# Kernel optimization log

Measured on AMD Instinct MI355X. Metric: run time of the kernel, lower is better.

## Reference

```python
import jax, jax.numpy as jnp
import numpy as np

T, B, I, H, O = 2048, 128, 128, 512, 128


def setup_inputs() -> dict:
    key = jax.random.key(0)
    ks = jax.random.split(key, 8)
    s = 0.05  # keep tanh out of hard saturation
    return {
        "input_seq": jax.random.randint(ks[0], (T, B), 0, I),
        "emb": jax.random.normal(ks[1], (I, I), jnp.float32),
        "Wxh_w": jax.random.normal(ks[2], (H, I), jnp.float32) * s,
        "Wxh_b": jax.random.normal(ks[3], (H,), jnp.float32) * s,
        "Whh_w": jax.random.normal(ks[4], (H, H), jnp.float32) * s,
        "Whh_b": jax.random.normal(ks[5], (H,), jnp.float32) * s,
        "dec_w": jax.random.normal(ks[6], (O, H), jnp.float32) * s,
        "dec_b": jax.random.normal(ks[7], (O,), jnp.float32) * s,
    }


def reference(input_seq, emb, Wxh_w, Wxh_b, Whh_w, Whh_b, dec_w, dec_b):
    x = emb[input_seq]                                   # [T, B, I]
    # input projection is h-independent: hoist out of the recurrence
    xh = jnp.einsum("tbi,hi->tbh", x, Wxh_w) + Wxh_b    # [T, B, H]

    def step(h, xt):
        # torch: res = tanh(Whh(h) + Wxh(x1)); self.h = res.detach()
        res = jnp.tanh(h @ Whh_w.T + Whh_b + xt)         # [B, H]
        return jax.lax.stop_gradient(res), res

    h0 = jnp.zeros((x.shape[1], Whh_w.shape[0]), x.dtype)
    _, out = jax.lax.scan(step, h0, xh)                  # [T, B, H]
    return out @ dec_w.T + dec_b                         # [T, B, O]
```

## Files before the change

kernel.cpp:

```cpp
#include <hip/hip_runtime.h>


#define TT 2048
#define BB 128
#define HH 512
#define OO 128
#define MAGIC 123456.0f
#define NLDG 18

typedef _Float16 h2_t __attribute__((ext_vector_type(2)));
typedef unsigned int u32x4 __attribute__((ext_vector_type(4)));
union UF { unsigned int u; float f; h2_t h; unsigned short us[2]; };

__device__ __forceinline__ unsigned int packf16(float a, float b) {
  UF r; r.h[0] = (_Float16)a; r.h[1] = (_Float16)b; return r.u;
}
__device__ __forceinline__ float dot2a(unsigned int a, unsigned int b, float c) {
  UF x, y; x.u = a; y.u = b;
#if __has_builtin(__builtin_amdgcn_fdot2)
  return __builtin_amdgcn_fdot2(x.h, y.h, c, false);
#else
  return fmaf((float)x.h[1], (float)y.h[1], fmaf((float)x.h[0], (float)y.h[0], c));
#endif
}
__device__ __forceinline__ unsigned short f16bits(float x) {
  UF r; r.h[0] = (_Float16)x; r.h[1] = (_Float16)0.f; return r.us[0];
}
__device__ __forceinline__ float f16tof(unsigned short u) {
  UF r; r.us[0] = u; r.us[1] = 0; return (float)r.h[0];
}
__device__ __forceinline__ float tanh_fast(float x) {
  float e = __expf(2.0f * x);
  return 1.0f - 2.0f / (e + 1.0f);
}
__device__ __forceinline__ float sanz(float x) {
  return (x >= -1e20f && x <= 1e20f) ? x : 0.f;
}
__device__ __forceinline__ unsigned int rdlane(unsigned int v, int l) {
#if __has_builtin(__builtin_amdgcn_readlane)
  return (unsigned int)__builtin_amdgcn_readlane((int)v, l);
#else
  return (unsigned int)__shfl((int)v, l, 64);
#endif
}

extern "C" __global__ void k_init(float* __restrict__ mk) {
  if (threadIdx.x < 8) mk[threadIdx.x] = 0.f;
}

extern "C" __global__ __launch_bounds__(512)
void k_pre(const float* __restrict__ emb, const float* __restrict__ wxh,
           const float* __restrict__ bxh, const float* __restrict__ bhh,
           float* __restrict__ P, float* __restrict__ mk) {
  const int id = blockIdx.x;
  const int j = threadIdx.x;
  const float4* er = (const float4*)(emb + id * 128);
  const float4* wr = (const float4*)(wxh + j * 128);
  float acc = 0.f;
  #pragma unroll
  for (int c = 0; c < 32; ++c) {
    const float4 e = er[c], w = wr[c];
    acc = fmaf(e.x, w.x, fmaf(e.y, w.y, fmaf(e.z, w.z, fmaf(e.w, w.w, acc))));
  }
  P[id * HH + j] = acc + bxh[j] + bhh[j];
  if (id == 0 && j == 0) mk[0] = MAGIC;
}

extern "C" __global__ __launch_bounds__(256)
void k_pack(const float* __restrict__ whh, unsigned int* __restrict__ wpack) {
  const int row = blockIdx.x;
  const int pd = threadIdx.x;
  const float2 w = *(const float2*)(whh + row * 512 + 2 * pd);
  wpack[row * 256 + pd] = packf16(w.x, w.y);
}

extern "C" __global__ __launch_bounds__(256)
void k_packd(const float* __restrict__ dw, uint4* __restrict__ decP4) {
  const int id = blockIdx.x * 256 + threadIdx.x;
  const int c4 = id >> 7, o = id & 127;
  const float* src = dw + o * 512 + 8 * c4;
  uint4 v;
  v.x = packf16(src[0], src[1]);
  v.y = packf16(src[2], src[3]);
  v.z = packf16(src[4], src[5]);
  v.w = packf16(src[6], src[7]);
  decP4[id] = v;
}

#define LOADBLK7(PTR, W0, W1, W2, W3, W4, W5, W6)             \
  asm volatile(                                               \
    "global_load_dwordx4 %0, %7, off\n\t"                     \
    "global_load_dwordx4 %1, %7, off offset:16\n\t"           \
    "global_load_dwordx4 %2, %7, off offset:32\n\t"           \
    "global_load_dwordx4 %3, %7, off offset:48\n\t"           \
    "global_load_dwordx4 %4, %7, off offset:64\n\t"           \
    "global_load_dwordx4 %5, %7, off offset:80\n\t"           \
    "global_load_dwordx4 %6, %7, off offset:96\n\t"           \
    "s_waitcnt vmcnt(0)"                                      \
    : "=&v"(W0), "=&v"(W1), "=&v"(W2), "=&v"(W3),             \
      "=&v"(W4), "=&v"(W5), "=&v"(W6)                         \
    : "v"(PTR))
#define LOADBLK4(PTR, W0, W1, W2, W3)                         \
  asm volatile(                                               \
    "global_load_dwordx4 %0, %4, off\n\t"                     \
    "global_load_dwordx4 %1, %4, off offset:16\n\t"           \
    "global_load_dwordx4 %2, %4, off offset:32\n\t"           \
    "global_load_dwordx4 %3, %4, off offset:48\n\t"           \
    "s_waitcnt vmcnt(0)"                                      \
    : "=&v"(W0), "=&v"(W1), "=&v"(W2), "=&v"(W3)              \
    : "v"(PTR))

#define GSTEP(W4, g)                                    \
  {                                                     \
    a0 = dot2a((W4).x, rdlane(hv.x, (g)), a0);          \
    a1 = dot2a((W4).y, rdlane(hv.y, (g)), a1);          \
    a2 = dot2a((W4).z, rdlane(hv.z, (g)), a2);          \
    a3 = dot2a((W4).w, rdlane(hv.w, (g)), a3);          \
  }

#define WL(X) \
  X(0) X(1) X(2) X(3) X(4) X(5) X(6) X(7) X(8) X(9) \
  X(10) X(11) X(12) X(13) X(14) X(15) X(16) X(17) X(18) X(19) \
  X(20) X(21) X(22) X(23) X(24) X(25) X(26) X(27) X(28) X(29) \
  X(30) X(31) X(32) X(33) X(34) X(35) X(36) X(37) X(38) X(39) \
  X(40) X(41) X(42) X(43) X(44) X(45)
#define DECLW(i) u32x4 w_##i;
#define USEW(i) GSTEP(w_##i, i)

extern "C" __global__
__attribute__((amdgpu_flat_work_group_size(512, 512), amdgpu_waves_per_eu(2, 2)))
void k_rec(const int* __restrict__ idx, const float* __restrict__ P,
           const unsigned int* __restrict__ wpack,
           float* __restrict__ hstate, unsigned short* __restrict__ ring16,
           float* __restrict__ mk, int t0, int nT) {
  extern __shared__ __align__(16) unsigned char smem[];
  u32x4* wl4 = (u32x4*)smem;
  unsigned short* hb16 = (unsigned short*)(smem + NLDG * 512 * 16);
  const uint4* hb4 = (const uint4*)hb16;
  const int tid = threadIdx.x;
  const int b = blockIdx.x;
  const int lane = tid & 63;
  if (t0 == 0 && b == 0 && tid == 0) mk[1] = MAGIC;

  const u32x4* wp = (const u32x4*)(wpack + (size_t)tid * 256);
  #pragma unroll
  for (int s = 0; s < NLDG; ++s) wl4[s * 512 + tid] = wp[46 + s];

  WL(DECLW)
  LOADBLK7(wp +  0, w_0,  w_1,  w_2,  w_3,  w_4,  w_5,  w_6);
  LOADBLK7(wp +  7, w_7,  w_8,  w_9,  w_10, w_11, w_12, w_13);
  LOADBLK7(wp + 14, w_14, w_15, w_16, w_17, w_18, w_19, w_20);
  LOADBLK7(wp + 21, w_21, w_22, w_23, w_24, w_25, w_26, w_27);
  LOADBLK7(wp + 28, w_28, w_29, w_30, w_31, w_32, w_33, w_34);
  LOADBLK7(wp + 35, w_35, w_36, w_37, w_38, w_39, w_40, w_41);
  LOADBLK4(wp + 42, w_42, w_43, w_44, w_45);

  const float h0 = (t0 == 0) ? 0.f : hstate[b * HH + tid];
  hb16[tid] = f16bits(h0);
  float hlast = h0;
  __syncthreads();

  for (int tl = 0; tl < nT; ++tl) {
    const int rb = tl & 1, wb = rb ^ 1;
    const int id = idx[(t0 + tl) * BB + b];
    const float pj = P[id * HH + tid];
    const uint4 hv = hb4[rb * 64 + lane];
    float a0 = 0.f, a1 = 0.f, a2 = 0.f, a3 = 0.f;
    #pragma unroll
    for (int s = 0; s < NLDG; ++s) {
      const u32x4 w4 = wl4[s * 512 + tid];
      GSTEP(w4, 46 + s);
    }
    WL(USEW)
    float s = a0 + a1 + a2 + a3 + pj;
    s = fminf(fmaxf(s, -30.f), 30.f);
    const float hvf = tanh_fast(s);
    const unsigned short h16 = f16bits(hvf);
    hb16[wb * 512 + tid] = h16;
    ring16[((size_t)tl * BB + b) * HH + tid] = h16;
    hlast = hvf;
    __syncthreads();
  }
  hstate[b * HH + tid] = hlast;
  if (t0 == 0 && b == 0 && tid == 0) mk[2] = MAGIC;
}

extern "C" __global__ __launch_bounds__(512)
void k_chk(const int* __restrict__ idx, const float* __restrict__ P,
           const unsigned int* __restrict__ wpack,
           const unsigned short* __restrict__ ring16, float* __restrict__ mk) {
  __shared__ unsigned short h1s[512];
  const int j = threadIdx.x;
  h1s[j] = ring16[j];
  __syncthreads();
  {
    const float pj = P[idx[0] * HH + j];
    const float s = fminf(fmaxf(pj, -30.f), 30.f);
    const float d = fabsf(f16tof(h1s[j]) - f16tof(f16bits(tanh_fast(s))));
    if (d > 0.02f) mk[5] = 7.f;
  }
  {
    const unsigned int* wr = wpack + (size_t)j * 256;
    const unsigned int* hp = (const unsigned int*)h1s;
    float a0 = 0.f, a1 = 0.f, a2 = 0.f, a3 = 0.f;
    for (int g = 0; g < 64; ++g) {
      a0 = dot2a(wr[4 * g + 0], hp[4 * g + 0], a0);
      a1 = dot2a(wr[4 * g + 1], hp[4 * g + 1], a1);
      a2 = dot2a(wr[4 * g + 2], hp[4 * g + 2], a2);
      a3 = dot2a(wr[4 * g + 3], hp[4 * g + 3], a3);
    }
    const float pj = P[idx[BB] * HH + j];
    const float s = fminf(fmaxf((a0 + a1) + (a2 + a3) + pj, -30.f), 30.f);
    const float d = fabsf(f16tof(ring16[BB * HH + j]) - f16tof(f16bits(tanh_fast(s))));
    if (d > 0.02f) mk[4] = 7.f;
  }
}

extern "C" __global__ __launch_bounds__(512)
void k_dec(const uint4* __restrict__ ring4, const uint4* __restrict__ decP4,
           const float* __restrict__ decb, float* __restrict__ out,
           float* __restrict__ mk, int t0) {
  extern __shared__ __align__(16) unsigned char smem[];
  uint4* hl4 = (uint4*)smem;
  const int tid = threadIdx.x;
  const size_t r0 = (size_t)blockIdx.x * 64;
  #pragma unroll
  for (int i = 0; i < 8; ++i) {
    const int u = i * 512 + tid;
    hl4[u] = ring4[(r0 + (u >> 6)) * 64 + (u & 63)];
  }
  __syncthreads();
  const int oq = tid & 31, tq = tid >> 5;
  float acc[4][4];
  #pragma unroll
  for (int r = 0; r < 4; ++r)
    #pragma unroll
    for (int s = 0; s < 4; ++s) acc[r][s] = 0.f;
  #pragma unroll 2
  for (int c4 = 0; c4 < 64; ++c4) {
    uint4 h4[4], d4[4];
    #pragma unroll
    for (int s = 0; s < 4; ++s) h4[s] = hl4[(tq + 16 * s) * 64 + c4];
    #pragma unroll
    for (int r = 0; r < 4; ++r) d4[r] = decP4[c4 * 128 + oq + 32 * r];
    #pragma unroll
    for (int r = 0; r < 4; ++r)
      #pragma unroll
      for (int s = 0; s < 4; ++s) {
        acc[r][s] = dot2a(d4[r].x, h4[s].x, acc[r][s]);
        acc[r][s] = dot2a(d4[r].y, h4[s].y, acc[r][s]);
        acc[r][s] = dot2a(d4[r].z, h4[s].z, acc[r][s]);
        acc[r][s] = dot2a(d4[r].w, h4[s].w, acc[r][s]);
      }
  }
  #pragma unroll
  for (int r = 0; r < 4; ++r) {
    const float db = decb[oq + 32 * r];
    #pragma unroll
    for (int s = 0; s < 4; ++s) {
      const size_t g = r0 + tq + 16 * s;
      out[((size_t)t0 * BB + g) * OO + oq + 32 * r] = sanz(acc[r][s] + db);
    }
  }
  if (t0 == 0 && blockIdx.x == 0 && tid == 0) mk[3] = MAGIC;
}

extern "C" __global__ void k_probe(const float* __restrict__ mk, float* __restrict__ out,
                                   int wsTooSmall) {
  if (wsTooSmall)     { out[0] = 100000.f; return; }
  if (mk[0] != MAGIC) { out[0] = 200000.f; return; }
  if (mk[1] != MAGIC) { out[0] = 300000.f; return; }
  if (mk[2] != MAGIC) { out[0] = 400000.f; return; }
  if (mk[3] != MAGIC) { out[0] = 500000.f; return; }
  if (mk[5] == 7.f)   { out[0] = 600000.f; return; }
  if (mk[4] == 7.f)   { out[0] = 700000.f; return; }
}

extern "C" void kernel_launch(void* const* d_in, const int* in_sizes, int n_in,
                              void* d_out, int out_size, void* d_ws, size_t ws_size,
                              hipStream_t stream) {
  (void)in_sizes; (void)n_in; (void)out_size;
  const int* idx = (const int*)d_in[0];
  const float* emb = (const float*)d_in[1];
  const float* wxh = (const float*)d_in[2];
  const float* bxh = (const float*)d_in[3];
  const float* whh = (const float*)d_in[4];
  const float* bhh = (const float*)d_in[5];
  const float* dw  = (const float*)d_in[6];
  const float* db  = (const float*)d_in[7];
  float* out = (float*)d_out;

  char* ws = (char*)d_ws;
  float* P = (float*)ws;
  float* hstate = (float*)(ws + (256 << 10));
  float* mk = (float*)(ws + (512 << 10));
  unsigned int* wpack = (unsigned int*)(ws + (516 << 10));
  uint4* decP4 = (uint4*)(ws + (1076 << 10));
  unsigned short* ring16 = (unsigned short*)(ws + (1204 << 10));

  int chunkT = 0;
  const int opts[8] = {2048, 1024, 768, 512, 256, 128, 32, 8};
  for (int i = 0; i < 8; ++i) {
    const size_t need = (size_t)(1204 << 10) + (size_t)opts[i] * BB * HH * 2;
    if (ws_size >= need) { chunkT = opts[i]; break; }
  }
  if (chunkT == 0) {
    k_probe<<<1, 1, 0, stream>>>(nullptr, out, 1);
    return;
  }

  const int ldsRec = NLDG * 512 * 16 + 2048;
  const int ldsDec = 64 * 64 * 16;
  (void)hipFuncSetAttribute(reinterpret_cast<const void*>(k_rec),
                            hipFuncAttributeMaxDynamicSharedMemorySize, ldsRec);
  (void)hipFuncSetAttribute(reinterpret_cast<const void*>(k_dec),
                            hipFuncAttributeMaxDynamicSharedMemorySize, ldsDec);

  k_init<<<1, 64, 0, stream>>>(mk);
  k_pre<<<128, 512, 0, stream>>>(emb, wxh, bxh, bhh, P, mk);
  k_pack<<<512, 256, 0, stream>>>(whh, wpack);
  k_packd<<<32, 256, 0, stream>>>(dw, decP4);
  bool first = true;
  for (int t0 = 0; t0 < TT; t0 += chunkT) {
    k_rec<<<BB, 512, ldsRec, stream>>>(idx, P, wpack, hstate, ring16, mk, t0, chunkT);
    if (first) {
      k_chk<<<1, 512, 0, stream>>>(idx, P, wpack, ring16, mk);
      first = false;
    }
    k_dec<<<chunkT * 2, 512, ldsDec, stream>>>((const uint4*)ring16, decP4, db, out, mk, t0);
  }
  k_probe<<<1, 1, 0, stream>>>(mk, out, 0);
}
```

Before: 4.953 ms.

## Stream recurrent weights from L2 each step instead of holding them in registers

```diff
diff --git a/kernel.cpp b/kernel.cpp
--- a/kernel.cpp
+++ b/kernel.cpp
@@ -6,7 +6,8 @@
 #define HH 512
 #define OO 128
 #define MAGIC 123456.0f
-#define NLDG 18
+#define NLDSG 19
+#define NSTRG 45
 
 typedef _Float16 h2_t __attribute__((ext_vector_type(2)));
 typedef unsigned int u32x4 __attribute__((ext_vector_type(4)));
@@ -72,6 +73,14 @@
   const int pd = threadIdx.x;
   const float2 w = *(const float2*)(whh + row * 512 + 2 * pd);
   wpack[row * 256 + pd] = packf16(w.x, w.y);
+}
+
+extern "C" __global__ __launch_bounds__(512)
+void k_packS(const unsigned int* __restrict__ wpack, u32x4* __restrict__ wstr4) {
+  const int g = blockIdx.x;
+  const int t = threadIdx.x;
+  const u32x4* src = (const u32x4*)wpack + (size_t)t * 64 + g;
+  wstr4[(size_t)g * 512 + t] = *src;
 }
 
 extern "C" __global__ __launch_bounds__(256)
@@ -87,29 +96,6 @@
   decP4[id] = v;
 }
 
-#define LOADBLK7(PTR, W0, W1, W2, W3, W4, W5, W6)             \
-  asm volatile(                                               \
-    "global_load_dwordx4 %0, %7, off\n\t"                     \
-    "global_load_dwordx4 %1, %7, off offset:16\n\t"           \
-    "global_load_dwordx4 %2, %7, off offset:32\n\t"           \
-    "global_load_dwordx4 %3, %7, off offset:48\n\t"           \
-    "global_load_dwordx4 %4, %7, off offset:64\n\t"           \
-    "global_load_dwordx4 %5, %7, off offset:80\n\t"           \
-    "global_load_dwordx4 %6, %7, off offset:96\n\t"           \
-    "s_waitcnt vmcnt(0)"                                      \
-    : "=&v"(W0), "=&v"(W1), "=&v"(W2), "=&v"(W3),             \
-      "=&v"(W4), "=&v"(W5), "=&v"(W6)                         \
-    : "v"(PTR))
-#define LOADBLK4(PTR, W0, W1, W2, W3)                         \
-  asm volatile(                                               \
-    "global_load_dwordx4 %0, %4, off\n\t"                     \
-    "global_load_dwordx4 %1, %4, off offset:16\n\t"           \
-    "global_load_dwordx4 %2, %4, off offset:32\n\t"           \
-    "global_load_dwordx4 %3, %4, off offset:48\n\t"           \
-    "s_waitcnt vmcnt(0)"                                      \
-    : "=&v"(W0), "=&v"(W1), "=&v"(W2), "=&v"(W3)              \
-    : "v"(PTR))
-
 #define GSTEP(W4, g)                                    \
   {                                                     \
     a0 = dot2a((W4).x, rdlane(hv.x, (g)), a0);          \
@@ -118,42 +104,24 @@
     a3 = dot2a((W4).w, rdlane(hv.w, (g)), a3);          \
   }
 
-#define WL(X) \
-  X(0) X(1) X(2) X(3) X(4) X(5) X(6) X(7) X(8) X(9) \
-  X(10) X(11) X(12) X(13) X(14) X(15) X(16) X(17) X(18) X(19) \
-  X(20) X(21) X(22) X(23) X(24) X(25) X(26) X(27) X(28) X(29) \
-  X(30) X(31) X(32) X(33) X(34) X(35) X(36) X(37) X(38) X(39) \
-  X(40) X(41) X(42) X(43) X(44) X(45)
-#define DECLW(i) u32x4 w_##i;
-#define USEW(i) GSTEP(w_##i, i)
-
 extern "C" __global__
 __attribute__((amdgpu_flat_work_group_size(512, 512), amdgpu_waves_per_eu(2, 2)))
 void k_rec(const int* __restrict__ idx, const float* __restrict__ P,
-           const unsigned int* __restrict__ wpack,
+           const u32x4* __restrict__ wstr4,
            float* __restrict__ hstate, unsigned short* __restrict__ ring16,
            float* __restrict__ mk, int t0, int nT) {
   extern __shared__ __align__(16) unsigned char smem[];
   u32x4* wl4 = (u32x4*)smem;
-  unsigned short* hb16 = (unsigned short*)(smem + NLDG * 512 * 16);
+  unsigned short* hb16 = (unsigned short*)(smem + NLDSG * 512 * 16);
   const uint4* hb4 = (const uint4*)hb16;
   const int tid = threadIdx.x;
   const int b = blockIdx.x;
   const int lane = tid & 63;
   if (t0 == 0 && b == 0 && tid == 0) mk[1] = MAGIC;
 
-  const u32x4* wp = (const u32x4*)(wpack + (size_t)tid * 256);
-  #pragma unroll
-  for (int s = 0; s < NLDG; ++s) wl4[s * 512 + tid] = wp[46 + s];
-
-  WL(DECLW)
-  LOADBLK7(wp +  0, w_0,  w_1,  w_2,  w_3,  w_4,  w_5,  w_6);
-  LOADBLK7(wp +  7, w_7,  w_8,  w_9,  w_10, w_11, w_12, w_13);
-  LOADBLK7(wp + 14, w_14, w_15, w_16, w_17, w_18, w_19, w_20);
-  LOADBLK7(wp + 21, w_21, w_22, w_23, w_24, w_25, w_26, w_27);
-  LOADBLK7(wp + 28, w_28, w_29, w_30, w_31, w_32, w_33, w_34);
-  LOADBLK7(wp + 35, w_35, w_36, w_37, w_38, w_39, w_40, w_41);
-  LOADBLK4(wp + 42, w_42, w_43, w_44, w_45);
+  #pragma unroll
+  for (int s = 0; s < NLDSG; ++s)
+    wl4[s * 512 + tid] = wstr4[(size_t)(NSTRG + s) * 512 + tid];
 
   const float h0 = (t0 == 0) ? 0.f : hstate[b * HH + tid];
   hb16[tid] = f16bits(h0);
@@ -167,11 +135,15 @@
     const uint4 hv = hb4[rb * 64 + lane];
     float a0 = 0.f, a1 = 0.f, a2 = 0.f, a3 = 0.f;
     #pragma unroll
-    for (int s = 0; s < NLDG; ++s) {
+    for (int s = 0; s < NLDSG; ++s) {
       const u32x4 w4 = wl4[s * 512 + tid];
-      GSTEP(w4, 46 + s);
-    }
-    WL(USEW)
+      GSTEP(w4, NSTRG + s);
+    }
+    #pragma unroll
+    for (int g = 0; g < NSTRG; ++g) {
+      const u32x4 w4 = wstr4[(size_t)g * 512 + tid];
+      GSTEP(w4, g);
+    }
     float s = a0 + a1 + a2 + a3 + pj;
     s = fminf(fmaxf(s, -30.f), 30.f);
     const float hvf = tanh_fast(s);
@@ -295,13 +267,14 @@
   float* hstate = (float*)(ws + (256 << 10));
   float* mk = (float*)(ws + (512 << 10));
   unsigned int* wpack = (unsigned int*)(ws + (516 << 10));
-  uint4* decP4 = (uint4*)(ws + (1076 << 10));
-  unsigned short* ring16 = (unsigned short*)(ws + (1204 << 10));
+  u32x4* wstr4 = (u32x4*)(ws + (1028 << 10));
+  uint4* decP4 = (uint4*)(ws + (1540 << 10));
+  unsigned short* ring16 = (unsigned short*)(ws + (1668 << 10));
 
   int chunkT = 0;
   const int opts[8] = {2048, 1024, 768, 512, 256, 128, 32, 8};
   for (int i = 0; i < 8; ++i) {
-    const size_t need = (size_t)(1204 << 10) + (size_t)opts[i] * BB * HH * 2;
+    const size_t need = (size_t)(1668 << 10) + (size_t)opts[i] * BB * HH * 2;
     if (ws_size >= need) { chunkT = opts[i]; break; }
   }
   if (chunkT == 0) {
@@ -309,7 +282,7 @@
     return;
   }
 
-  const int ldsRec = NLDG * 512 * 16 + 2048;
+  const int ldsRec = NLDSG * 512 * 16 + 2048;
   const int ldsDec = 64 * 64 * 16;
   (void)hipFuncSetAttribute(reinterpret_cast<const void*>(k_rec),
                             hipFuncAttributeMaxDynamicSharedMemorySize, ldsRec);
@@ -319,10 +292,11 @@
   k_init<<<1, 64, 0, stream>>>(mk);
   k_pre<<<128, 512, 0, stream>>>(emb, wxh, bxh, bhh, P, mk);
   k_pack<<<512, 256, 0, stream>>>(whh, wpack);
+  k_packS<<<64, 512, 0, stream>>>(wpack, wstr4);
   k_packd<<<32, 256, 0, stream>>>(dw, decP4);
   bool first = true;
   for (int t0 = 0; t0 < TT; t0 += chunkT) {
-    k_rec<<<BB, 512, ldsRec, stream>>>(idx, P, wpack, hstate, ring16, mk, t0, chunkT);
+    k_rec<<<BB, 512, ldsRec, stream>>>(idx, P, wstr4, hstate, ring16, mk, t0, chunkT);
     if (first) {
       k_chk<<<1, 512, 0, stream>>>(idx, P, wpack, ring16, mk);
       first = false;
```

Measured after the change: 5.049 ms. No clear change (+1.9%).
